# Kernel optimization log

Measured on AMD Instinct MI355X. Metric: run time of the kernel, lower is better.

## Reference

```python
import jax, jax.numpy as jnp
import numpy as np

# db4 (Daubechies-4) lowpass decomposition filter, L = 8 taps
DB4 = np.array([0.23037781330885523, 0.7148465705525415, 0.6308807679295904,
                -0.027983769416983849, -0.18703481171888114, 0.030841381835986965,
                0.032883011666982945, -0.010597401784997278], dtype=np.float32)


def setup_inputs() -> dict:
    key = jax.random.key(0)
    x = jax.random.normal(key, (4, 256, 256, 256), dtype=jnp.float32)
    h = jnp.asarray(DB4)
    return {"x": x, "h": h}


def _corr_valid(u, f):
    # u: [..., T], f: [L]; cross-correlation with VALID padding (== tf.nn.conv1d)
    L = f.shape[0]
    B = int(np.prod(u.shape[:-1]))
    out = jax.lax.conv_general_dilated(
        u.reshape(B, 1, u.shape[-1]), f.reshape(1, 1, L),
        window_strides=(1,), padding='VALID',
        dimension_numbers=('NCW', 'OIW', 'NCW'))
    return out.reshape(u.shape[:-1] + (out.shape[-1],))


def _recon_axis(s, w, h0, h1, axis):
    # s, w: scale / wavelet coefficient halves, same shape; recon along `axis`
    L = h0.shape[0]
    P = (L - 2) // 2 + 1  # number of periodic-wrap samples (= L//2 for even L)
    x = jnp.stack([s, w])                      # [2, ...]
    x = jnp.moveaxis(x, axis + 1, -1)          # bring recon axis to last
    N = x.shape[-1]
    # periodic extension (cyclic gather of last P) then drop first -> len N+P-1
    x = jnp.concatenate([x[..., N - P:], x], axis=-1)[..., 1:]
    # zero-interleaved upsample: [0, x0, 0, x1, ...], then one trailing zero -> len 2N+L-1
    up = jnp.stack([jnp.zeros_like(x), x], axis=-1).reshape(x.shape[:-1] + (-1,))
    up = jnp.pad(up, [(0, 0)] * (up.ndim - 1) + [(0, 1)])
    y = _corr_valid(up[0], h0) + _corr_valid(up[1], h1)  # [..., 2N]
    return jnp.moveaxis(y, -1, axis)


def reference(x, h):
    h0 = h[::-1]                                        # reversed lowpass
    sign = jnp.where(jnp.arange(h.shape[0]) % 2 == 0, -1.0, 1.0).astype(h.dtype)
    h1 = sign * h                                       # QMF highpass (double reverse cancels)
    out = x
    for axis in range(1, x.ndim):
        s, w = jnp.split(out, 2, axis=axis)
        out = _recon_axis(s, w, h0, h1, axis)
    return out
```

## Files before the change

kernel.cpp:

```cpp
#include <hip/hip_runtime.h>


#define FILT_DECL(h)                                          \
  const float a0 = h[6], a1 = h[4], a2 = h[2], a3 = h[0];     \
  const float b0 = h[7], b1 = h[5], b2 = h[3], b3 = h[1];     \
  const float c0 = h[1], c1 = h[3], c2 = h[5], c3 = h[7];     \
  const float d0 = -h[0], d1 = -h[2], d2 = -h[4], d3 = -h[6];

#define Y0(s0,s1,s2,s3,w0,w1,w2,w3)                                        \
  fmaf(w3, c3, fmaf(w2, c2, fmaf(w1, c1, fmaf(w0, c0,                      \
  fmaf(s3, a3, fmaf(s2, a2, fmaf(s1, a1, s0 * a0)))))))
#define Y1(s0,s1,s2,s3,w0,w1,w2,w3)                                        \
  fmaf(w3, d3, fmaf(w2, d2, fmaf(w1, d1, fmaf(w0, d0,                      \
  fmaf(s3, b3, fmaf(s2, b2, fmaf(s1, b1, s0 * b0)))))))

__global__ __launch_bounds__(256) void wav_axis1_s(const float* __restrict__ in,
                                                   float* __restrict__ tmp,
                                                   const float* __restrict__ h) {
  const int inner = blockIdx.x * 256 + threadIdx.x;
  const int m0 = blockIdx.y * 64;
  const size_t base = (size_t)blockIdx.z * (256u * 65536u) + (unsigned)inner;
  const float* __restrict__ ps = in + base;
  const float* __restrict__ pw = in + base + (size_t)128 * 65536;
  float* __restrict__ po = tmp + base;
  FILT_DECL(h)
  float s0 = __builtin_nontemporal_load(&ps[(size_t)((m0 - 3) & 127) * 65536]);
  float s1 = __builtin_nontemporal_load(&ps[(size_t)((m0 - 2) & 127) * 65536]);
  float s2 = __builtin_nontemporal_load(&ps[(size_t)((m0 - 1) & 127) * 65536]);
  float w0 = __builtin_nontemporal_load(&pw[(size_t)((m0 - 3) & 127) * 65536]);
  float w1 = __builtin_nontemporal_load(&pw[(size_t)((m0 - 2) & 127) * 65536]);
  float w2 = __builtin_nontemporal_load(&pw[(size_t)((m0 - 1) & 127) * 65536]);
  for (int m = m0; m < m0 + 64; ++m) {
    const float s3 = __builtin_nontemporal_load(&ps[(size_t)m * 65536]);
    const float w3 = __builtin_nontemporal_load(&pw[(size_t)m * 65536]);
    po[(size_t)(2 * m) * 65536] = Y0(s0, s1, s2, s3, w0, w1, w2, w3);
    po[(size_t)(2 * m + 1) * 65536] = Y1(s0, s1, s2, s3, w0, w1, w2, w3);
    s0 = s1; s1 = s2; s2 = s3;
    w0 = w1; w1 = w2; w2 = w3;
  }
}

__global__ __launch_bounds__(256, 4) void wav_t23(const float* __restrict__ tmp,
                                                  float* __restrict__ out,
                                                  const float* __restrict__ hg) {
  __shared__ float lb[38 * 137];
  const int t = threadIdx.x;
  const int d2t = blockIdx.x & 7;
  const int d3t = blockIdx.x >> 3;
  const size_t slice = blockIdx.y;
  const float* __restrict__ src = tmp + slice * 65536;
  FILT_DECL(hg)
  const int mb2 = 16 * d2t - 3;
  const int mb3 = 64 * d3t - 3;

  for (int e = t; e < 38 * 134; e += 256) {
    const int i2 = e / 134, i3 = e - i2 * 134;
    const int g2 = (i2 < 19) ? ((mb2 + i2) & 127) : (128 + ((mb2 + i2 - 19) & 127));
    const int g3 = (i3 < 67) ? ((mb3 + i3) & 127) : (128 + ((mb3 + i3 - 67) & 127));
    lb[i2 * 137 + i3] = src[g2 * 256 + g3];
  }
  __syncthreads();

  if (t < 134) {
    float S[19], W[19];
#pragma unroll
    for (int i = 0; i < 19; ++i) S[i] = lb[i * 137 + t];
#pragma unroll
    for (int i = 0; i < 19; ++i) W[i] = lb[(19 + i) * 137 + t];
#pragma unroll
    for (int p = 0; p < 16; ++p) {
      lb[p * 137 + t]        = Y0(S[p], S[p+1], S[p+2], S[p+3], W[p], W[p+1], W[p+2], W[p+3]);
      lb[(19 + p) * 137 + t] = Y1(S[p], S[p+1], S[p+2], S[p+3], W[p], W[p+1], W[p+2], W[p+3]);
    }
  }
  __syncthreads();

  const int r = t >> 3, pc = t & 7;
  const int prow = ((r & 1) ? (19 + (r >> 1)) : (r >> 1)) * 137;
  const int cc0 = 8 * pc;
  float S[11], W[11];
#pragma unroll
  for (int i = 0; i < 11; ++i) S[i] = lb[prow + cc0 + i];
#pragma unroll
  for (int i = 0; i < 11; ++i) W[i] = lb[prow + 67 + cc0 + i];
  float y[16];
#pragma unroll
  for (int q = 0; q < 8; ++q) {
    y[2*q]   = Y0(S[q], S[q+1], S[q+2], S[q+3], W[q], W[q+1], W[q+2], W[q+3]);
    y[2*q+1] = Y1(S[q], S[q+1], S[q+2], S[q+3], W[q], W[q+1], W[q+2], W[q+3]);
  }
  float* __restrict__ dst = out + slice * 65536
      + (size_t)(32 * d2t + r) * 256 + 128 * d3t + 16 * pc;
#pragma unroll
  for (int v = 0; v < 4; ++v)
    *reinterpret_cast<float4*>(dst + 4 * v) =
        make_float4(y[4*v], y[4*v+1], y[4*v+2], y[4*v+3]);
}

__global__ __launch_bounds__(256) void wav_axis1(const float* __restrict__ in,
                                                 float* __restrict__ out,
                                                 const float* __restrict__ h) {
  const int inner = blockIdx.x * 256 + threadIdx.x;
  const int m0 = blockIdx.y * 64;
  const size_t base = (size_t)blockIdx.z * (256u * 65536u) + (unsigned)inner;
  const float* __restrict__ ps = in + base;
  const float* __restrict__ pw = in + base + (size_t)128 * 65536;
  float* __restrict__ po = out + base;
  FILT_DECL(h)
  float s0 = ps[(size_t)((m0 - 3) & 127) * 65536];
  float s1 = ps[(size_t)((m0 - 2) & 127) * 65536];
  float s2 = ps[(size_t)((m0 - 1) & 127) * 65536];
  float w0 = pw[(size_t)((m0 - 3) & 127) * 65536];
  float w1 = pw[(size_t)((m0 - 2) & 127) * 65536];
  float w2 = pw[(size_t)((m0 - 1) & 127) * 65536];
  for (int m = m0; m < m0 + 64; ++m) {
    const float s3 = ps[(size_t)m * 65536];
    const float w3 = pw[(size_t)m * 65536];
    po[(size_t)(2 * m) * 65536] = Y0(s0, s1, s2, s3, w0, w1, w2, w3);
    po[(size_t)(2 * m + 1) * 65536] = Y1(s0, s1, s2, s3, w0, w1, w2, w3);
    s0 = s1; s1 = s2; s2 = s3;
    w0 = w1; w1 = w2; w2 = w3;
  }
}

__global__ __launch_bounds__(256) void wav_axis2(float* __restrict__ buf,
                                                 const float* __restrict__ h) {
  __shared__ float tile[256][32];
  const int t = threadIdx.x;
  const int c = t & 31;
  const int g = t >> 5;
  const size_t slice = (size_t)(blockIdx.x >> 3);
  const int col0 = (blockIdx.x & 7) * 32;
  float* __restrict__ p = buf + slice * 65536 + col0;
#pragma unroll
  for (int i = 0; i < 32; ++i) {
    const int rr = i * 8 + g;
    tile[rr][c] = p[rr * 256 + c];
  }
  __syncthreads();
  FILT_DECL(h)
  const int m0 = g * 16;
  float s0 = tile[(m0 - 3) & 127][c];
  float s1 = tile[(m0 - 2) & 127][c];
  float s2 = tile[(m0 - 1) & 127][c];
  float w0 = tile[128 + ((m0 - 3) & 127)][c];
  float w1 = tile[128 + ((m0 - 2) & 127)][c];
  float w2 = tile[128 + ((m0 - 1) & 127)][c];
#pragma unroll
  for (int m = m0; m < m0 + 16; ++m) {
    const float s3 = tile[m][c];
    const float w3 = tile[128 + m][c];
    p[(2 * m) * 256 + c] = Y0(s0, s1, s2, s3, w0, w1, w2, w3);
    p[(2 * m + 1) * 256 + c] = Y1(s0, s1, s2, s3, w0, w1, w2, w3);
    s0 = s1; s1 = s2; s2 = s3;
    w0 = w1; w1 = w2; w2 = w3;
  }
}

__global__ __launch_bounds__(256) void wav_axis3(float* __restrict__ buf,
                                                 const float* __restrict__ h) {
  __shared__ float tile[512];
  const int t = threadIdx.x;
  float* __restrict__ p = buf + (size_t)blockIdx.x * 512;
  tile[t] = p[t];
  tile[256 + t] = p[256 + t];
  __syncthreads();
  FILT_DECL(h)
  const int rr = t >> 7;
  const int m = t & 127;
  const float* __restrict__ line = tile + rr * 256;
  const float s0 = line[(m - 3) & 127];
  const float s1 = line[(m - 2) & 127];
  const float s2 = line[(m - 1) & 127];
  const float s3 = line[m];
  const float w0 = line[128 + ((m - 3) & 127)];
  const float w1 = line[128 + ((m - 2) & 127)];
  const float w2 = line[128 + ((m - 1) & 127)];
  const float w3 = line[128 + m];
  float2 y;
  y.x = Y0(s0, s1, s2, s3, w0, w1, w2, w3);
  y.y = Y1(s0, s1, s2, s3, w0, w1, w2, w3);
  *reinterpret_cast<float2*>(p + rr * 256 + 2 * m) = y;
}

extern "C" void kernel_launch(void* const* d_in, const int* in_sizes, int n_in,
                              void* d_out, int out_size, void* d_ws, size_t ws_size,
                              hipStream_t stream) {
  const float* x = (const float*)d_in[0];
  const float* h = (const float*)d_in[1];
  float* out = (float*)d_out;
  const size_t need = (size_t)4 * 256 * 256 * 256 * 4;

  if (ws_size >= need) {
    float* tmp = (float*)d_ws;
    wav_axis1_s<<<dim3(256, 2, 4), 256, 0, stream>>>(x, tmp, h);
    wav_t23<<<dim3(16, 1024), 256, 0, stream>>>(tmp, out, h);
  } else {
    wav_axis1<<<dim3(256, 2, 4), 256, 0, stream>>>(x, out, h);
    wav_axis2<<<dim3(8192), 256, 0, stream>>>(out, h);
    wav_axis3<<<dim3(131072), 256, 0, stream>>>(out, h);
  }
}
```

Before: 244.7 us.

## Widen fused axis-2/3 tile to full rows, removing axis-3 halo reload

The fused axis-2/axis-3 reconstruction kernel now processes full 256-wide rows per block with 512 threads, instead of 64-column chunks with halos. The axis-3 periodic wrap becomes an index mask within shared memory, so the redundant halo loads and the div/mod index arithmetic go away, and global loads are contiguous row segments with precomputed row offsets. All threads take part in the axis-2 pass rather than only 134. The larger shared tile and 512-thread blocks may reduce occupancy.

```diff
diff --git a/kernel.cpp b/kernel.cpp
--- a/kernel.cpp
+++ b/kernel.cpp
@@ -40,61 +40,67 @@
   }
 }
 
-__global__ __launch_bounds__(256, 4) void wav_t23(const float* __restrict__ tmp,
-                                                  float* __restrict__ out,
-                                                  const float* __restrict__ hg) {
-  __shared__ float lb[38 * 137];
+__global__ __launch_bounds__(512, 8) void wav_t23w(const float* __restrict__ tmp,
+                                                   float* __restrict__ out,
+                                                   const float* __restrict__ hg) {
+  __shared__ float lb[38 * 257];
+  __shared__ int gg2[38];
   const int t = threadIdx.x;
-  const int d2t = blockIdx.x & 7;
-  const int d3t = blockIdx.x >> 3;
+  const int d2t = blockIdx.x;
   const size_t slice = blockIdx.y;
   const float* __restrict__ src = tmp + slice * 65536;
   FILT_DECL(hg)
   const int mb2 = 16 * d2t - 3;
-  const int mb3 = 64 * d3t - 3;
-
-  for (int e = t; e < 38 * 134; e += 256) {
-    const int i2 = e / 134, i3 = e - i2 * 134;
-    const int g2 = (i2 < 19) ? ((mb2 + i2) & 127) : (128 + ((mb2 + i2 - 19) & 127));
-    const int g3 = (i3 < 67) ? ((mb3 + i3) & 127) : (128 + ((mb3 + i3 - 67) & 127));
-    lb[i2 * 137 + i3] = src[g2 * 256 + g3];
-  }
-  __syncthreads();
-
-  if (t < 134) {
-    float S[19], W[19];
-#pragma unroll
-    for (int i = 0; i < 19; ++i) S[i] = lb[i * 137 + t];
-#pragma unroll
-    for (int i = 0; i < 19; ++i) W[i] = lb[(19 + i) * 137 + t];
-#pragma unroll
-    for (int p = 0; p < 16; ++p) {
-      lb[p * 137 + t]        = Y0(S[p], S[p+1], S[p+2], S[p+3], W[p], W[p+1], W[p+2], W[p+3]);
-      lb[(19 + p) * 137 + t] = Y1(S[p], S[p+1], S[p+2], S[p+3], W[p], W[p+1], W[p+2], W[p+3]);
+
+  if (t < 38) {
+    const int g2 = (t < 19) ? ((mb2 + t) & 127) : (128 + ((mb2 + t - 19) & 127));
+    gg2[t] = g2 << 8;
+  }
+  __syncthreads();
+
+  for (int k = 0; k < 19; ++k) {
+    const int e = t + 512 * k;
+    const int i2 = e >> 8, i3 = e & 255;
+    lb[i2 * 257 + i3] = src[gg2[i2] + i3];
+  }
+  __syncthreads();
+
+  {
+    const int j = t >> 1, p0 = (t & 1) * 8;
+    float S[11], W[11];
+#pragma unroll
+    for (int i = 0; i < 11; ++i) S[i] = lb[(p0 + i) * 257 + j];
+#pragma unroll
+    for (int i = 0; i < 11; ++i) W[i] = lb[(19 + p0 + i) * 257 + j];
+#pragma unroll
+    for (int q = 0; q < 8; ++q) {
+      const int p = p0 + q;
+      lb[p * 257 + j]        = Y0(S[q], S[q+1], S[q+2], S[q+3], W[q], W[q+1], W[q+2], W[q+3]);
+      lb[(19 + p) * 257 + j] = Y1(S[q], S[q+1], S[q+2], S[q+3], W[q], W[q+1], W[q+2], W[q+3]);
     }
   }
   __syncthreads();
 
-  const int r = t >> 3, pc = t & 7;
-  const int prow = ((r & 1) ? (19 + (r >> 1)) : (r >> 1)) * 137;
-  const int cc0 = 8 * pc;
+  const int r = t >> 4, m0 = (t & 15) * 8;
+  const int prow = ((r & 1) ? (19 + (r >> 1)) : (r >> 1)) * 257;
   float S[11], W[11];
 #pragma unroll
-  for (int i = 0; i < 11; ++i) S[i] = lb[prow + cc0 + i];
-#pragma unroll
-  for (int i = 0; i < 11; ++i) W[i] = lb[prow + 67 + cc0 + i];
-  float y[16];
-#pragma unroll
-  for (int q = 0; q < 8; ++q) {
-    y[2*q]   = Y0(S[q], S[q+1], S[q+2], S[q+3], W[q], W[q+1], W[q+2], W[q+3]);
-    y[2*q+1] = Y1(S[q], S[q+1], S[q+2], S[q+3], W[q], W[q+1], W[q+2], W[q+3]);
+  for (int i = 0; i < 11; ++i) {
+    const int cs = (m0 + i - 3) & 127;
+    S[i] = lb[prow + cs];
+    W[i] = lb[prow + 128 + cs];
   }
   float* __restrict__ dst = out + slice * 65536
-      + (size_t)(32 * d2t + r) * 256 + 128 * d3t + 16 * pc;
-#pragma unroll
-  for (int v = 0; v < 4; ++v)
-    *reinterpret_cast<float4*>(dst + 4 * v) =
-        make_float4(y[4*v], y[4*v+1], y[4*v+2], y[4*v+3]);
+      + (size_t)(32 * d2t + r) * 256 + 16 * (t & 15);
+#pragma unroll
+  for (int g = 0; g < 4; ++g) {
+    float4 y;
+    y.x = Y0(S[2*g],   S[2*g+1], S[2*g+2], S[2*g+3], W[2*g],   W[2*g+1], W[2*g+2], W[2*g+3]);
+    y.y = Y1(S[2*g],   S[2*g+1], S[2*g+2], S[2*g+3], W[2*g],   W[2*g+1], W[2*g+2], W[2*g+3]);
+    y.z = Y0(S[2*g+1], S[2*g+2], S[2*g+3], S[2*g+4], W[2*g+1], W[2*g+2], W[2*g+3], W[2*g+4]);
+    y.w = Y1(S[2*g+1], S[2*g+2], S[2*g+3], S[2*g+4], W[2*g+1], W[2*g+2], W[2*g+3], W[2*g+4]);
+    *reinterpret_cast<float4*>(dst + 4 * g) = y;
+  }
 }
 
 __global__ __launch_bounds__(256) void wav_axis1(const float* __restrict__ in,
@@ -194,7 +200,7 @@
   if (ws_size >= need) {
     float* tmp = (float*)d_ws;
     wav_axis1_s<<<dim3(256, 2, 4), 256, 0, stream>>>(x, tmp, h);
-    wav_t23<<<dim3(16, 1024), 256, 0, stream>>>(tmp, out, h);
+    wav_t23w<<<dim3(8, 1024), 512, 0, stream>>>(tmp, out, h);
   } else {
     wav_axis1<<<dim3(256, 2, 4), 256, 0, stream>>>(x, out, h);
     wav_axis2<<<dim3(8192), 256, 0, stream>>>(out, h);
```

New measurement: 223.5 us. -8.7%, faster.

## Restructure fused axis-2/3 kernel as row-streaming with packed FMA and small LDS ring

Applied to the files above, without the earlier changes.

Replaces the 2D-tiled axis-2/3 kernel with one that streams axis-2 rows through registers (one thread per column, sliding window). Each group of 4 input rows produces 8 filtered rows, which are staged into a small padded shared buffer with periodic halo duplicates and then filtered along axis 3 with float4 stores. Both filters use packed 2-wide FMA so the Y0/Y1 outputs are computed together. This removes the large halo-overlap reloads of the old tile scheme, at the cost of two barriers per step, fewer blocks (2048), and a serial dependency chain per thread.

```diff
diff --git a/kernel.cpp b/kernel.cpp
--- a/kernel.cpp
+++ b/kernel.cpp
@@ -1,5 +1,7 @@
 #include <hip/hip_runtime.h>
 
+
+typedef float f32x2 __attribute__((ext_vector_type(2)));
 
 #define FILT_DECL(h)                                          \
   const float a0 = h[6], a1 = h[4], a2 = h[2], a3 = h[0];     \
@@ -13,6 +15,8 @@
 #define Y1(s0,s1,s2,s3,w0,w1,w2,w3)                                        \
   fmaf(w3, d3, fmaf(w2, d2, fmaf(w1, d1, fmaf(w0, d0,                      \
   fmaf(s3, b3, fmaf(s2, b2, fmaf(s1, b1, s0 * b0)))))))
+
+#define PKFMA(s, k, acc) __builtin_elementwise_fma((f32x2){(s),(s)}, (k), (acc))
 
 __global__ __launch_bounds__(256) void wav_axis1_s(const float* __restrict__ in,
                                                    float* __restrict__ tmp,
@@ -40,61 +44,94 @@
   }
 }
 
-__global__ __launch_bounds__(256, 4) void wav_t23(const float* __restrict__ tmp,
-                                                  float* __restrict__ out,
-                                                  const float* __restrict__ hg) {
-  __shared__ float lb[38 * 137];
+#define RSTR 264
+__global__ __launch_bounds__(256) void wav_t23r(const float* __restrict__ tmp,
+                                                float* __restrict__ out,
+                                                const float* __restrict__ hg) {
+  __shared__ __align__(16) float rb[8 * RSTR];
   const int t = threadIdx.x;
-  const int d2t = blockIdx.x & 7;
-  const int d3t = blockIdx.x >> 3;
-  const size_t slice = blockIdx.y;
-  const float* __restrict__ src = tmp + slice * 65536;
+  const size_t slice = blockIdx.x >> 1;
+  const int m0 = (blockIdx.x & 1) << 6;
+  const float* __restrict__ ps = tmp + slice * 65536 + t;
+  const float* __restrict__ pw = tmp + slice * 65536 + 32768 + t;
+  float* __restrict__ outs = out + slice * 65536;
   FILT_DECL(hg)
-  const int mb2 = 16 * d2t - 3;
-  const int mb3 = 64 * d3t - 3;
-
-  for (int e = t; e < 38 * 134; e += 256) {
-    const int i2 = e / 134, i3 = e - i2 * 134;
-    const int g2 = (i2 < 19) ? ((mb2 + i2) & 127) : (128 + ((mb2 + i2 - 19) & 127));
-    const int g3 = (i3 < 67) ? ((mb3 + i3) & 127) : (128 + ((mb3 + i3 - 67) & 127));
-    lb[i2 * 137 + i3] = src[g2 * 256 + g3];
-  }
-  __syncthreads();
-
-  if (t < 134) {
-    float S[19], W[19];
-#pragma unroll
-    for (int i = 0; i < 19; ++i) S[i] = lb[i * 137 + t];
-#pragma unroll
-    for (int i = 0; i < 19; ++i) W[i] = lb[(19 + i) * 137 + t];
-#pragma unroll
-    for (int p = 0; p < 16; ++p) {
-      lb[p * 137 + t]        = Y0(S[p], S[p+1], S[p+2], S[p+3], W[p], W[p+1], W[p+2], W[p+3]);
-      lb[(19 + p) * 137 + t] = Y1(S[p], S[p+1], S[p+2], S[p+3], W[p], W[p+1], W[p+2], W[p+3]);
+  const f32x2 AB0 = {a0, b0}, AB1 = {a1, b1}, AB2 = {a2, b2}, AB3 = {a3, b3};
+  const f32x2 CD0 = {c0, d0}, CD1 = {c1, d1}, CD2 = {c2, d2}, CD3 = {c3, d3};
+  const int phys = t + ((t < 128) ? 3 : 7);
+  const int hcol = (t >= 125 && t < 128) ? (t - 125)
+                 : ((t >= 253) ? (t - 121) : -1);
+  const int lr = t >> 5;
+  const int p0 = (t & 31) << 2;
+
+  float S0 = ps[((m0 - 3) & 127) << 8];
+  float S1 = ps[((m0 - 2) & 127) << 8];
+  float S2 = ps[((m0 - 1) & 127) << 8];
+  float W0 = pw[((m0 - 3) & 127) << 8];
+  float W1 = pw[((m0 - 2) & 127) << 8];
+  float W2 = pw[((m0 - 1) & 127) << 8];
+
+  for (int ss = 0; ss < 16; ++ss) {
+    const int ms = m0 + 4 * ss;
+#pragma unroll
+    for (int q = 0; q < 4; ++q) {
+      const float S3 = ps[(ms + q) << 8];
+      const float W3 = pw[(ms + q) << 8];
+      f32x2 acc = (f32x2){S0, S0} * AB0;
+      acc = PKFMA(S1, AB1, acc);
+      acc = PKFMA(S2, AB2, acc);
+      acc = PKFMA(S3, AB3, acc);
+      acc = PKFMA(W0, CD0, acc);
+      acc = PKFMA(W1, CD1, acc);
+      acc = PKFMA(W2, CD2, acc);
+      acc = PKFMA(W3, CD3, acc);
+      rb[(2 * q) * RSTR + phys] = acc.x;
+      rb[(2 * q + 1) * RSTR + phys] = acc.y;
+      if (hcol >= 0) {
+        rb[(2 * q) * RSTR + hcol] = acc.x;
+        rb[(2 * q + 1) * RSTR + hcol] = acc.y;
+      }
+      S0 = S1; S1 = S2; S2 = S3;
+      W0 = W1; W1 = W2; W2 = W3;
     }
-  }
-  __syncthreads();
-
-  const int r = t >> 3, pc = t & 7;
-  const int prow = ((r & 1) ? (19 + (r >> 1)) : (r >> 1)) * 137;
-  const int cc0 = 8 * pc;
-  float S[11], W[11];
-#pragma unroll
-  for (int i = 0; i < 11; ++i) S[i] = lb[prow + cc0 + i];
-#pragma unroll
-  for (int i = 0; i < 11; ++i) W[i] = lb[prow + 67 + cc0 + i];
-  float y[16];
-#pragma unroll
-  for (int q = 0; q < 8; ++q) {
-    y[2*q]   = Y0(S[q], S[q+1], S[q+2], S[q+3], W[q], W[q+1], W[q+2], W[q+3]);
-    y[2*q+1] = Y1(S[q], S[q+1], S[q+2], S[q+3], W[q], W[q+1], W[q+2], W[q+3]);
-  }
-  float* __restrict__ dst = out + slice * 65536
-      + (size_t)(32 * d2t + r) * 256 + 128 * d3t + 16 * pc;
-#pragma unroll
-  for (int v = 0; v < 4; ++v)
-    *reinterpret_cast<float4*>(dst + 4 * v) =
-        make_float4(y[4*v], y[4*v+1], y[4*v+2], y[4*v+3]);
+    __syncthreads();
+
+    const int rbase = lr * RSTR;
+    float S[8], W[8];
+    {
+      const float4 sa = *reinterpret_cast<const float4*>(&rb[rbase + p0]);
+      const float4 sb = *reinterpret_cast<const float4*>(&rb[rbase + p0 + 4]);
+      S[0]=sa.x; S[1]=sa.y; S[2]=sa.z; S[3]=sa.w;
+      S[4]=sb.x; S[5]=sb.y; S[6]=sb.z; S[7]=sb.w;
+      const float4 wa = *reinterpret_cast<const float4*>(&rb[rbase + 132 + p0]);
+      const float4 wb = *reinterpret_cast<const float4*>(&rb[rbase + 132 + p0 + 4]);
+      W[0]=wa.x; W[1]=wa.y; W[2]=wa.z; W[3]=wa.w;
+      W[4]=wb.x; W[5]=wb.y; W[6]=wb.z; W[7]=wb.w;
+    }
+    float* __restrict__ dst = outs + (size_t)(2 * ms + lr) * 256 + 2 * p0;
+#pragma unroll
+    for (int g = 0; g < 2; ++g) {
+      const int k = 2 * g;
+      f32x2 eA = (f32x2){S[k], S[k]} * AB0;
+      eA = PKFMA(S[k+1], AB1, eA);
+      eA = PKFMA(S[k+2], AB2, eA);
+      eA = PKFMA(S[k+3], AB3, eA);
+      eA = PKFMA(W[k],   CD0, eA);
+      eA = PKFMA(W[k+1], CD1, eA);
+      eA = PKFMA(W[k+2], CD2, eA);
+      eA = PKFMA(W[k+3], CD3, eA);
+      f32x2 eB = (f32x2){S[k+1], S[k+1]} * AB0;
+      eB = PKFMA(S[k+2], AB1, eB);
+      eB = PKFMA(S[k+3], AB2, eB);
+      eB = PKFMA(S[k+4], AB3, eB);
+      eB = PKFMA(W[k+1], CD0, eB);
+      eB = PKFMA(W[k+2], CD1, eB);
+      eB = PKFMA(W[k+3], CD2, eB);
+      eB = PKFMA(W[k+4], CD3, eB);
+      *reinterpret_cast<float4*>(dst + 4 * g) = make_float4(eA.x, eA.y, eB.x, eB.y);
+    }
+    __syncthreads();
+  }
 }
 
 __global__ __launch_bounds__(256) void wav_axis1(const float* __restrict__ in,
@@ -194,7 +231,7 @@
   if (ws_size >= need) {
     float* tmp = (float*)d_ws;
     wav_axis1_s<<<dim3(256, 2, 4), 256, 0, stream>>>(x, tmp, h);
-    wav_t23<<<dim3(16, 1024), 256, 0, stream>>>(tmp, out, h);
+    wav_t23r<<<dim3(2048), 256, 0, stream>>>(tmp, out, h);
   } else {
     wav_axis1<<<dim3(256, 2, 4), 256, 0, stream>>>(x, out, h);
     wav_axis2<<<dim3(8192), 256, 0, stream>>>(out, h);
```

Measured after the change: 232.7 us. -4.9%, faster.
